# Kernel optimization log

Hardware: AMD Instinct MI355X
Metric: run time of the kernel (lower is better)

## Reference

```python
import jax, jax.numpy as jnp
import numpy as np

B, D_IN, D_H, D_F = 65536, 256, 1024, 512


def _linear_init(key, fan_in, fan_out):
    # torch.nn.Linear default: U(-1/sqrt(fan_in), 1/sqrt(fan_in))
    bound = 1.0 / np.sqrt(fan_in)
    kw, kb = jax.random.split(key)
    W = jax.random.uniform(kw, (fan_in, fan_out), minval=-bound, maxval=bound, dtype=jnp.float32)
    b = jax.random.uniform(kb, (fan_out,), minval=-bound, maxval=bound, dtype=jnp.float32)
    return W, b


def setup_inputs() -> dict:
    key = jax.random.key(0)
    ks = jax.random.split(key, 8)
    obs = jax.random.normal(ks[0], (B, D_IN), dtype=jnp.float32)
    # columns 2:4 must be one-hot: [1,0] -> expert b, [0,1] -> expert c
    tag = jax.random.randint(ks[1], (B,), 0, 2).astype(jnp.float32)
    onehot = jnp.stack([tag, 1.0 - tag], axis=1)  # [B, 2]
    obs = obs.at[:, 2:4].set(onehot)
    inp = {"obs": obs}
    for i, name in enumerate(("b", "c", "p")):
        k1, k2 = jax.random.split(ks[2 + i])
        W1, b1 = _linear_init(k1, D_IN, D_H)
        W2, b2 = _linear_init(k2, D_H, D_F)
        inp[f"W1_{name}"] = W1
        inp[f"b1_{name}"] = b1
        inp[f"W2_{name}"] = W2
        inp[f"b2_{name}"] = b2
    return inp


def _mlp(x, W1, b1, W2, b2):
    # Linear -> ReLU -> Linear (tianshou-style MLP, flatten_input=False)
    return jax.nn.relu(x @ W1 + b1) @ W2 + b2


def reference(obs, W1_b, b1_b, W2_b, b2_b, W1_c, b1_c, W2_c, b2_c, W1_p, b1_p, W2_p, b2_p):
    # Vectorized form of the per-row Python loop: compute both experts and the
    # shared branch on the full batch, then select per row by the one-hot tag.
    out_b = _mlp(obs, W1_b, b1_b, W2_b, b2_b)  # [B, D_F]
    out_c = _mlp(obs, W1_c, b1_c, W2_c, b2_c)  # [B, D_F]
    out_p = _mlp(obs, W1_p, b1_p, W2_p, b2_p)  # [B, D_F]
    is_b = (obs[:, 2:3] == 1.0) & (obs[:, 3:4] == 0.0)  # [B, 1]
    expert = jnp.where(is_b, out_b, out_c)
    return jnp.concatenate([expert, out_p], axis=-1)  # [B, 2*D_F]
```

## Files before the change

### kernel.cpp

```cpp
#include <hip/hip_runtime.h>
#include <hip/hip_bf16.h>

#define DIN 256
#define DH  1024
#define DF  512
#define NROWS 65536

#define WS_WTS   0
#define WS_PB    4718592
#define WS_PC    4980736
#define WS_CNT   5242880
#define WS_OFFS  5243904

typedef __attribute__((ext_vector_type(8))) short bf16x8;
typedef __attribute__((ext_vector_type(4))) float f32x4;

__device__ __forceinline__ unsigned short f2b(float f) {
    union { float f; unsigned u; } v; v.f = f;
    unsigned r = v.u + 0x7FFFu + ((v.u >> 16) & 1u);
    return (unsigned short)(r >> 16);
}

__device__ __forceinline__ void gll16(const void* g, void* l) {
    __builtin_amdgcn_global_load_lds(
        (const __attribute__((address_space(1))) void*)g,
        (__attribute__((address_space(3))) void*)l, 16, 0, 0);
}

__global__ __launch_bounds__(256) void transpose_to_bf16(
        const float* __restrict__ src, unsigned short* __restrict__ dst,
        int K, int N) {
    __shared__ float tile[64][65];
    int k0 = blockIdx.x * 64, n0 = blockIdx.y * 64;
    int t = threadIdx.x;
    for (int i = 0; i < 16; ++i) {
        int idx = t + i * 256;
        int kk = idx >> 6, nn = idx & 63;
        tile[kk][nn] = src[(size_t)(k0 + kk) * N + (n0 + nn)];
    }
    __syncthreads();
    for (int i = 0; i < 16; ++i) {
        int idx = t + i * 256;
        int nn = idx >> 6, kk = idx & 63;
        dst[(size_t)(n0 + nn) * K + (k0 + kk)] = f2b(tile[kk][nn]);
    }
}

__device__ __forceinline__ int row_tag(const float* obs, int row) {
    float c2 = obs[(size_t)row * DIN + 2];
    float c3 = obs[(size_t)row * DIN + 3];
    return (c2 == 1.0f && c3 == 0.0f) ? 1 : 0;
}

__global__ __launch_bounds__(256) void tag_count(const float* __restrict__ obs,
                                                 int* __restrict__ cnt) {
    int t = threadIdx.x;
    int tag = row_tag(obs, blockIdx.x * 256 + t);
    unsigned long long m = __ballot(tag);
    __shared__ int wc[4];
    if ((t & 63) == 0) wc[t >> 6] = __popcll(m);
    __syncthreads();
    if (t == 0) cnt[blockIdx.x] = wc[0] + wc[1] + wc[2] + wc[3];
}

__global__ __launch_bounds__(256) void scan256(const int* __restrict__ cnt,
                                               int* __restrict__ offs) {
    __shared__ int s[256];
    int t = threadIdx.x;
    s[t] = cnt[t];
    __syncthreads();
    for (int d = 1; d < 256; d <<= 1) {
        int v = (t >= d) ? s[t - d] : 0;
        __syncthreads();
        s[t] += v;
        __syncthreads();
    }
    offs[t] = s[t] - cnt[t];
    if (t == 255) offs[256] = s[255];
}

__global__ __launch_bounds__(256) void fill_perm(const float* __restrict__ obs,
                                                 const int* __restrict__ offs,
                                                 int* __restrict__ pb,
                                                 int* __restrict__ pc) {
    int t = threadIdx.x, bid = blockIdx.x;
    int row = bid * 256 + t;
    int tag = row_tag(obs, row);
    unsigned long long m = __ballot(tag);
    __shared__ int wc[4];
    int lane = t & 63, wv = t >> 6;
    if (lane == 0) wc[wv] = __popcll(m);
    __syncthreads();
    int woff = 0;
    for (int i = 0; i < 4; ++i) if (i < wv) woff += wc[i];
    int lb = woff + __popcll(m & ((1ull << lane) - 1ull));
    int base_b = offs[bid];
    if (tag) pb[base_b + lb] = row;
    else     pc[bid * 256 - base_b + (t - lb)] = row;
}

__global__ __launch_bounds__(512, 2) void fused_mlp(
    const float* __restrict__ obs,
    const unsigned short* __restrict__ wts,
    const int* __restrict__ perm_b, const int* __restrict__ perm_c,
    const int* __restrict__ offs,
    const float* __restrict__ b1_0, const float* __restrict__ b2_0,
    const float* __restrict__ b1_1, const float* __restrict__ b2_1,
    const float* __restrict__ b1_2, const float* __restrict__ b2_2,
    float* __restrict__ out)
{
    extern __shared__ char lds[];
    char* ldsX  = lds;
    char* ldsW1 = lds + 65536;
    char* ldsQA = lds + 98304;
    char* ldsQB = lds + 114688;
    char* ldsH  = lds + 131072;
    float* ldsB1 = (float*)(lds + 147456);
    float* ldsB2 = (float*)(lds + 151552);
    int*  ldsPr  = (int*)(lds + 153600);

    const int ob = blockIdx.x;
    const int xcd = ob & 7, ii = ob >> 3;
    const int bid = (xcd == 0) ? ii : (129 + (xcd - 1) * 128 + ii);

    int branch, base, cnt;
    const int* perm;
    if (bid < 512) {
        branch = 2; base = bid * 128; cnt = NROWS; perm = nullptr;
    } else {
        int eb = bid - 512;
        int nb = offs[256];
        int nbb = (nb + 127) >> 7;
        int nc = NROWS - nb;
        int ncb = (nc + 127) >> 7;
        if (eb < nbb)            { branch = 0; base = eb * 128;         cnt = nb; perm = perm_b; }
        else if (eb < nbb + ncb) { branch = 1; base = (eb - nbb) * 128; cnt = nc; perm = perm_c; }
        else return;
    }

    const float* b1 = branch == 0 ? b1_0 : (branch == 1 ? b1_1 : b1_2);
    const float* b2 = branch == 0 ? b2_0 : (branch == 1 ? b2_1 : b2_2);
    const char* w1t = (const char*)(wts + (size_t)branch * (DH * DIN));
    const char* w2t = (const char*)(wts + (size_t)3 * DH * DIN + (size_t)branch * (DF * DH));

    const int t = threadIdx.x;
    const int lane = t & 63;
    const int w = t >> 6;
    const int l15 = lane & 15;
    const int g = lane >> 4;

    ldsB1[t] = b1[t];
    ldsB1[t + 512] = b1[t + 512];
    ldsB2[t] = b2[t];
    if (t < 128) {
        int gr = base + t;
        ldsPr[t] = (gr < cnt) ? (perm ? perm[gr] : gr) : -1;
    }
    #pragma unroll
    for (int i = 0; i < 16; ++i) {
        int idx = t + i * 512;
        int r = idx >> 6, c4 = idx & 63;
        int gr = base + r;
        int grow = gr < cnt ? gr : cnt - 1;
        if (perm) grow = perm[grow];
        f32x4 v = *(const f32x4*)(obs + (size_t)grow * DIN + c4 * 4);
        ushort4 p4;
        p4.x = f2b(v.x); p4.y = f2b(v.y); p4.z = f2b(v.z); p4.w = f2b(v.w);
        *(ushort4*)(ldsX + r * 512 + ((c4 * 8) ^ ((r & 7) << 4))) = p4;
    }
    #pragma unroll
    for (int i = 0; i < 4; ++i) {
        int slot = t + i * 512;
        int nl = slot >> 5, boff = (slot & 31) << 4;
        gll16(w1t + (size_t)nl * 512 + (boff ^ ((nl & 7) << 4)), ldsW1 + slot * 16);
    }
    __syncthreads();

    const int rg = w & 3, cg = w >> 2;
    const int wr = w >> 2, wc = w & 3;

    const int ar0 = rg * 32 + l15, ar1 = ar0 + 16;
    const int asw0 = (ar0 & 7) << 4, asw1 = (ar1 & 7) << 4;
    const int bn0 = cg * 32 + l15, bn1 = bn0 + 16;
    const int bsw0 = (bn0 & 7) << 4, bsw1 = (bn1 & 7) << 4;

    f32x4 acc[4][8];
    #pragma unroll
    for (int a = 0; a < 4; ++a)
        #pragma unroll
        for (int b = 0; b < 8; ++b)
            #pragma unroll
            for (int e = 0; e < 4; ++e) acc[a][b][e] = 0.0f;

    #define STAGE_Q(buf, q, hc_)                                               \
        {                                                                      \
            _Pragma("unroll")                                                  \
            for (int i = 0; i < 2; ++i) {                                      \
                int slot = t + i * 512;                                        \
                int nl = slot >> 3, boff = (slot & 7) << 4;                    \
                gll16(w2t + (size_t)((q) * 128 + nl) * 2048 + (hc_) * 128      \
                          + (boff ^ ((nl & 7) << 4)),                          \
                      (buf) + slot * 16);                                      \
            }                                                                  \
        }

    #define QUARTER_MFMA(buf, c0)                                              \
        {                                                                      \
            _Pragma("unroll")                                                  \
            for (int k2 = 0; k2 < 2; ++k2)                                     \
                _Pragma("unroll")                                              \
                for (int ct = 0; ct < 2; ++ct) {                               \
                    int fr = wc * 32 + ct * 16 + l15;                          \
                    bf16x8 bb = *(const bf16x8*)((buf) + fr * 128 +            \
                                 ((k2 * 64 + g * 16) ^ ((fr & 7) << 4)));      \
                    _Pragma("unroll")                                          \
                    for (int rt = 0; rt < 4; ++rt)                             \
                        acc[rt][(c0) + ct] = __builtin_amdgcn_mfma_f32_16x16x32_bf16( \
                            hA[rt][k2], bb, acc[rt][(c0) + ct], 0, 0, 0);      \
                }                                                              \
        }

    for (int hc = 0; hc < 16; ++hc) {
        STAGE_Q(ldsQA, 0, hc);
        f32x4 aH[2][2];
        #pragma unroll
        for (int a = 0; a < 2; ++a)
            #pragma unroll
            for (int b = 0; b < 2; ++b)
                #pragma unroll
                for (int e = 0; e < 4; ++e) aH[a][b][e] = 0.0f;
        __builtin_amdgcn_s_setprio(1);
        #pragma unroll
        for (int kk = 0; kk < 8; ++kk) {
            int kb = kk * 64 + g * 16;
            bf16x8 a0 = *(const bf16x8*)(ldsX  + ar0 * 512 + (kb ^ asw0));
            bf16x8 a1 = *(const bf16x8*)(ldsX  + ar1 * 512 + (kb ^ asw1));
            bf16x8 b0 = *(const bf16x8*)(ldsW1 + bn0 * 512 + (kb ^ bsw0));
            bf16x8 b1f = *(const bf16x8*)(ldsW1 + bn1 * 512 + (kb ^ bsw1));
            aH[0][0] = __builtin_amdgcn_mfma_f32_16x16x32_bf16(a0, b0,  aH[0][0], 0, 0, 0);
            aH[0][1] = __builtin_amdgcn_mfma_f32_16x16x32_bf16(a0, b1f, aH[0][1], 0, 0, 0);
            aH[1][0] = __builtin_amdgcn_mfma_f32_16x16x32_bf16(a1, b0,  aH[1][0], 0, 0, 0);
            aH[1][1] = __builtin_amdgcn_mfma_f32_16x16x32_bf16(a1, b1f, aH[1][1], 0, 0, 0);
        }
        __builtin_amdgcn_s_setprio(0);
        {
            float b1v0 = ldsB1[hc * 64 + cg * 32 + l15];
            float b1v1 = ldsB1[hc * 64 + cg * 32 + 16 + l15];
            #pragma unroll
            for (int art = 0; art < 2; ++art)
                #pragma unroll
                for (int bct = 0; bct < 2; ++bct) {
                    int col2 = (cg * 32 + bct * 16 + l15) * 2;
                    float bv = bct ? b1v1 : b1v0;
                    #pragma unroll
                    for (int r = 0; r < 4; ++r) {
                        int hrow = rg * 32 + art * 16 + g * 4 + r;
                        float vv = fmaxf(aH[art][bct][r] + bv, 0.0f);
                        *(unsigned short*)(ldsH + hrow * 128 + (col2 ^ ((hrow & 7) << 4))) = f2b(vv);
                    }
                }
        }
        __syncthreads();

        STAGE_Q(ldsQB, 1, hc);
        bf16x8 hA[4][2];
        #pragma unroll
        for (int rt = 0; rt < 4; ++rt)
            #pragma unroll
            for (int k2 = 0; k2 < 2; ++k2) {
                int hr = wr * 64 + rt * 16 + l15;
                hA[rt][k2] = *(const bf16x8*)(ldsH + hr * 128 + ((k2 * 64 + g * 16) ^ ((hr & 7) << 4)));
            }
        __builtin_amdgcn_s_setprio(1);
        QUARTER_MFMA(ldsQA, 0);
        __builtin_amdgcn_s_setprio(0);
        __syncthreads();

        STAGE_Q(ldsQA, 2, hc);
        __builtin_amdgcn_s_setprio(1);
        QUARTER_MFMA(ldsQB, 2);
        __builtin_amdgcn_s_setprio(0);
        __syncthreads();

        STAGE_Q(ldsQB, 3, hc);
        __builtin_amdgcn_s_setprio(1);
        QUARTER_MFMA(ldsQA, 4);
        __builtin_amdgcn_s_setprio(0);
        __syncthreads();

        if (hc < 15) {
            int nchunk = hc + 1;
            #pragma unroll
            for (int i = 0; i < 4; ++i) {
                int slot = t + i * 512;
                int nl = slot >> 5, boff = (slot & 31) << 4;
                gll16(w1t + (size_t)(nchunk * 64 + nl) * 512 + (boff ^ ((nl & 7) << 4)),
                      ldsW1 + slot * 16);
            }
        }
        __builtin_amdgcn_s_setprio(1);
        QUARTER_MFMA(ldsQB, 6);
        __builtin_amdgcn_s_setprio(0);
        __syncthreads();
    }

    int colq[8]; float b2v[8];
    #pragma unroll
    for (int q = 0; q < 8; ++q) {
        colq[q] = (q >> 1) * 128 + wc * 32 + (q & 1) * 16 + l15;
        b2v[q] = ldsB2[colq[q]];
    }
    const int cb = (branch == 2) ? DF : 0;
    #pragma unroll
    for (int rt = 0; rt < 4; ++rt)
        #pragma unroll
        for (int r = 0; r < 4; ++r) {
            int row = wr * 64 + rt * 16 + g * 4 + r;
            int prow = ldsPr[row];
            if (prow >= 0) {
                float* op = out + (size_t)prow * (2 * DF) + cb;
                #pragma unroll
                for (int q = 0; q < 8; ++q)
                    op[colq[q]] = acc[rt][q][r] + b2v[q];
            }
        }
}

extern "C" void kernel_launch(void* const* d_in, const int* in_sizes, int n_in,
                              void* d_out, int out_size, void* d_ws, size_t ws_size,
                              hipStream_t stream) {
    const float* obs = (const float*)d_in[0];
    const float* W1[3] = {(const float*)d_in[1], (const float*)d_in[5], (const float*)d_in[9]};
    const float* b1[3] = {(const float*)d_in[2], (const float*)d_in[6], (const float*)d_in[10]};
    const float* W2[3] = {(const float*)d_in[3], (const float*)d_in[7], (const float*)d_in[11]};
    const float* b2[3] = {(const float*)d_in[4], (const float*)d_in[8], (const float*)d_in[12]};

    char* ws = (char*)d_ws;
    unsigned short* wts = (unsigned short*)(ws + WS_WTS);
    int* pb   = (int*)(ws + WS_PB);
    int* pc   = (int*)(ws + WS_PC);
    int* cnt  = (int*)(ws + WS_CNT);
    int* offs = (int*)(ws + WS_OFFS);

    for (int br = 0; br < 3; ++br) {
        transpose_to_bf16<<<dim3(DIN / 64, DH / 64), 256, 0, stream>>>(
            W1[br], wts + (size_t)br * DH * DIN, DIN, DH);
        transpose_to_bf16<<<dim3(DH / 64, DF / 64), 256, 0, stream>>>(
            W2[br], wts + (size_t)3 * DH * DIN + (size_t)br * DF * DH, DH, DF);
    }
    tag_count<<<256, 256, 0, stream>>>(obs, cnt);
    scan256<<<1, 256, 0, stream>>>(cnt, offs);
    fill_perm<<<256, 256, 0, stream>>>(obs, offs, pb, pc);

    hipFuncSetAttribute((const void*)fused_mlp,
                        hipFuncAttributeMaxDynamicSharedMemorySize, 154112);
    fused_mlp<<<1025, 512, 154112, stream>>>(obs, wts, pb, pc, offs,
        b1[0], b2[0], b1[1], b2[1], b1[2], b2[2], (float*)d_out);
}
```

Baseline: 376.2 us.

## Split fused MLP into hidden and output kernels staged through workspace

Replaces the single fused MLP kernel with two kernels per pass. The first computes the bf16 hidden activations into a large workspace buffer. The second reads them back and computes the output GEMM with a 128x512 tile, scattering results to the permuted rows. The shared branch and the routed experts run as separate passes over a unified row permutation. This aims to lower LDS pressure and give the second GEMM larger register tiles, at the cost of writing and re-reading the hidden buffer (about 128MB per pass) through HBM. The old fused path remains as a fallback when the workspace is too small.

Result: slower. 450.1 us (+19.6%).

```diff
diff --git a/kernel.cpp b/kernel.cpp
--- a/kernel.cpp
+++ b/kernel.cpp
@@ -11,6 +11,9 @@
 #define WS_PC    4980736
 #define WS_CNT   5242880
 #define WS_OFFS  5243904
+#define WS_U     5248000
+#define WS_H     8388608ull
+#define WS_NEED  (8388608ull + 134742016ull)
 
 typedef __attribute__((ext_vector_type(8))) short bf16x8;
 typedef __attribute__((ext_vector_type(4))) float f32x4;
@@ -97,6 +100,300 @@
     int base_b = offs[bid];
     if (tag) pb[base_b + lb] = row;
     else     pc[bid * 256 - base_b + (t - lb)] = row;
+}
+
+__global__ __launch_bounds__(256) void fill_permU(const float* __restrict__ obs,
+                                                  const int* __restrict__ offs,
+                                                  int* __restrict__ U) {
+    int t = threadIdx.x, bid = blockIdx.x;
+    int row = bid * 256 + t;
+    int tag = row_tag(obs, row);
+    unsigned long long m = __ballot(tag);
+    __shared__ int wc[4];
+    int lane = t & 63, wv = t >> 6;
+    if (lane == 0) wc[wv] = __popcll(m);
+    __syncthreads();
+    int woff = 0;
+    for (int i = 0; i < 4; ++i) if (i < wv) woff += wc[i];
+    int lb = woff + __popcll(m & ((1ull << lane) - 1ull));
+    int base_b = offs[bid];
+    int nb = offs[256];
+    if (tag) U[base_b + lb] = row;
+    else     U[nb + bid * 256 - base_b + (t - lb)] = row;
+}
+
+__global__ __launch_bounds__(512, 1) void k1_hidden(
+    const float* __restrict__ obs, const unsigned short* __restrict__ wts,
+    const int* __restrict__ U, const int* __restrict__ offs,
+    const float* __restrict__ b1_0, const float* __restrict__ b1_1,
+    const float* __restrict__ b1_2,
+    unsigned short* __restrict__ H, int mode)
+{
+    extern __shared__ char lds[];
+    char* ldsX   = lds;
+    char* ldsW1a = lds + 65536;
+    char* ldsW1b = lds + 98304;
+    float* ldsB1 = (float*)(lds + 131072);
+
+    const int bid = blockIdx.x;
+    const int nb  = offs[256];
+    const int nc  = NROWS - nb;
+    const int nbp = (nb + 127) & ~127;
+    const int ncp = (nc + 127) & ~127;
+    const int evb = bid * 128;
+    int branch;
+    if (mode == 0) branch = 2;
+    else {
+        if (evb >= nbp + ncp) return;
+        branch = (evb < nbp) ? 0 : 1;
+    }
+    const float* b1g = branch == 0 ? b1_0 : (branch == 1 ? b1_1 : b1_2);
+    const char* w1t = (const char*)(wts + (size_t)branch * (DH * DIN));
+
+    const int t = threadIdx.x;
+    const int lane = t & 63;
+    const int w = t >> 6;
+    const int l15 = lane & 15;
+    const int g = lane >> 4;
+
+    ldsB1[t] = b1g[t];
+    ldsB1[t + 512] = b1g[t + 512];
+
+    #pragma unroll
+    for (int i = 0; i < 16; ++i) {
+        int idx = t + i * 512;
+        int r = idx >> 6, c4 = idx & 63;
+        int j = evb + r;
+        int grow;
+        if (mode == 0) grow = j;
+        else if (j < nbp) grow = U[j < nb ? j : nb - 1];
+        else { int ix = j - nbp; grow = U[nb + (ix < nc ? ix : nc - 1)]; }
+        f32x4 v = *(const f32x4*)(obs + (size_t)grow * DIN + c4 * 4);
+        ushort4 p4;
+        p4.x = f2b(v.x); p4.y = f2b(v.y); p4.z = f2b(v.z); p4.w = f2b(v.w);
+        *(ushort4*)(ldsX + r * 512 + ((c4 * 8) ^ ((r & 7) << 4))) = p4;
+    }
+    #pragma unroll
+    for (int i = 0; i < 4; ++i) {
+        int slot = t + i * 512;
+        int nl = slot >> 5, boff = (slot & 31) << 4;
+        gll16(w1t + (size_t)nl * 512 + (boff ^ ((nl & 7) << 4)), ldsW1a + slot * 16);
+    }
+    __syncthreads();
+
+    const int rg = w & 3, cg = w >> 2;
+    const int ar0 = rg * 32 + l15, ar1 = ar0 + 16;
+    const int asw0 = (ar0 & 7) << 4, asw1 = (ar1 & 7) << 4;
+    const int bn0 = cg * 32 + l15, bn1 = bn0 + 16;
+    const int bsw0 = (bn0 & 7) << 4, bsw1 = (bn1 & 7) << 4;
+    const size_t hb = (size_t)bid * 128;
+
+    for (int wch = 0; wch < 16; ++wch) {
+        const char* Wc = (wch & 1) ? ldsW1b : ldsW1a;
+        if (wch < 15) {
+            char* dst = (wch & 1) ? ldsW1a : ldsW1b;
+            #pragma unroll
+            for (int i = 0; i < 4; ++i) {
+                int slot = t + i * 512;
+                int nl = slot >> 5, boff = (slot & 31) << 4;
+                gll16(w1t + (size_t)((wch + 1) * 64 + nl) * 512 + (boff ^ ((nl & 7) << 4)),
+                      dst + slot * 16);
+            }
+        }
+        f32x4 aH[2][2];
+        #pragma unroll
+        for (int a = 0; a < 2; ++a)
+            #pragma unroll
+            for (int b = 0; b < 2; ++b)
+                #pragma unroll
+                for (int e = 0; e < 4; ++e) aH[a][b][e] = 0.0f;
+        __builtin_amdgcn_s_setprio(1);
+        #pragma unroll
+        for (int kk = 0; kk < 8; ++kk) {
+            int kb = kk * 64 + g * 16;
+            bf16x8 a0  = *(const bf16x8*)(ldsX + ar0 * 512 + (kb ^ asw0));
+            bf16x8 a1  = *(const bf16x8*)(ldsX + ar1 * 512 + (kb ^ asw1));
+            bf16x8 b0  = *(const bf16x8*)(Wc + bn0 * 512 + (kb ^ bsw0));
+            bf16x8 b1f = *(const bf16x8*)(Wc + bn1 * 512 + (kb ^ bsw1));
+            aH[0][0] = __builtin_amdgcn_mfma_f32_16x16x32_bf16(a0, b0,  aH[0][0], 0, 0, 0);
+            aH[0][1] = __builtin_amdgcn_mfma_f32_16x16x32_bf16(a0, b1f, aH[0][1], 0, 0, 0);
+            aH[1][0] = __builtin_amdgcn_mfma_f32_16x16x32_bf16(a1, b0,  aH[1][0], 0, 0, 0);
+            aH[1][1] = __builtin_amdgcn_mfma_f32_16x16x32_bf16(a1, b1f, aH[1][1], 0, 0, 0);
+        }
+        __builtin_amdgcn_s_setprio(0);
+        {
+            float b1v0 = ldsB1[wch * 64 + cg * 32 + l15];
+            float b1v1 = ldsB1[wch * 64 + cg * 32 + 16 + l15];
+            #pragma unroll
+            for (int art = 0; art < 2; ++art)
+                #pragma unroll
+                for (int bct = 0; bct < 2; ++bct) {
+                    float bv = bct ? b1v1 : b1v0;
+                    int hcol = wch * 64 + cg * 32 + bct * 16 + l15;
+                    #pragma unroll
+                    for (int r = 0; r < 4; ++r) {
+                        int hrow = rg * 32 + art * 16 + g * 4 + r;
+                        float vv = fmaxf(aH[art][bct][r] + bv, 0.0f);
+                        H[(hb + hrow) * DH + hcol] = f2b(vv);
+                    }
+                }
+        }
+        __syncthreads();
+    }
+}
+
+__global__ __launch_bounds__(512, 1) void k2_out(
+    const unsigned short* __restrict__ H, const unsigned short* __restrict__ wts,
+    const int* __restrict__ U, const int* __restrict__ offs,
+    const float* __restrict__ b2_0, const float* __restrict__ b2_1,
+    const float* __restrict__ b2_2,
+    float* __restrict__ out, int mode)
+{
+    extern __shared__ char lds[];
+    char* ldsHA  = lds;
+    char* ldsHB  = lds + 16384;
+    char* ldsW2A = lds + 32768;
+    char* ldsW2B = lds + 65536;
+    float* ldsB2 = (float*)(lds + 98304);
+    int*  ldsPr  = (int*)(lds + 100352);
+
+    const int bid = blockIdx.x;
+    const int nb  = offs[256];
+    const int nc  = NROWS - nb;
+    const int nbp = (nb + 127) & ~127;
+    const int ncp = (nc + 127) & ~127;
+    const int evb = bid * 128;
+    int branch;
+    if (mode == 0) branch = 2;
+    else {
+        if (evb >= nbp + ncp) return;
+        branch = (evb < nbp) ? 0 : 1;
+    }
+    const float* b2g = branch == 0 ? b2_0 : (branch == 1 ? b2_1 : b2_2);
+    const char* w2t = (const char*)(wts + (size_t)3 * DH * DIN + (size_t)branch * (DF * DH));
+
+    const int t = threadIdx.x;
+    const int lane = t & 63;
+    const int w = t >> 6;
+    const int l15 = lane & 15;
+    const int g = lane >> 4;
+
+    ldsB2[t] = b2g[t];
+    if (t < 128) {
+        int j = evb + t;
+        int pr;
+        if (mode == 0) pr = j;
+        else if (j < nbp) pr = U[j < nb ? j : nb - 1];
+        else { int ix = j - nbp; pr = U[nb + (ix < nc ? ix : nc - 1)]; }
+        ldsPr[t] = pr;
+    }
+    const size_t hb = (size_t)bid * 128;
+
+    #pragma unroll
+    for (int i = 0; i < 2; ++i) {
+        int slot = t + i * 512;
+        int nl = slot >> 3, boff = (slot & 7) << 4;
+        gll16((const char*)H + (hb + nl) * 2048 + (boff ^ ((nl & 7) << 4)),
+              ldsHA + slot * 16);
+    }
+    #pragma unroll
+    for (int i = 0; i < 4; ++i) {
+        int slot = t + i * 512;
+        int nl = slot >> 3, boff = (slot & 7) << 4;
+        gll16(w2t + (size_t)nl * 2048 + (boff ^ ((nl & 7) << 4)), ldsW2A + slot * 16);
+    }
+    __syncthreads();
+
+    const int wr = w >> 2, wc = w & 3;
+    f32x4 acc[4][8];
+    #pragma unroll
+    for (int a = 0; a < 4; ++a)
+        #pragma unroll
+        for (int b = 0; b < 8; ++b)
+            #pragma unroll
+            for (int e = 0; e < 4; ++e) acc[a][b][e] = 0.0f;
+
+    for (int ch = 0; ch < 16; ++ch) {
+        const char* Hc = (ch & 1) ? ldsHB : ldsHA;
+        #pragma unroll
+        for (int i = 0; i < 4; ++i) {
+            int slot = t + i * 512;
+            int nl = slot >> 3, boff = (slot & 7) << 4;
+            gll16(w2t + (size_t)(256 + nl) * 2048 + ch * 128 + (boff ^ ((nl & 7) << 4)),
+                  ldsW2B + slot * 16);
+        }
+        bf16x8 hA[4][2];
+        #pragma unroll
+        for (int rt = 0; rt < 4; ++rt)
+            #pragma unroll
+            for (int k2 = 0; k2 < 2; ++k2) {
+                int hr = wr * 64 + rt * 16 + l15;
+                hA[rt][k2] = *(const bf16x8*)(Hc + hr * 128 + ((k2 * 64 + g * 16) ^ ((hr & 7) << 4)));
+            }
+        __builtin_amdgcn_s_setprio(1);
+        #pragma unroll
+        for (int k2 = 0; k2 < 2; ++k2)
+            #pragma unroll
+            for (int ct = 0; ct < 4; ++ct) {
+                int fr = wc * 64 + ct * 16 + l15;
+                bf16x8 bb = *(const bf16x8*)(ldsW2A + fr * 128 + ((k2 * 64 + g * 16) ^ ((fr & 7) << 4)));
+                #pragma unroll
+                for (int rt = 0; rt < 4; ++rt)
+                    acc[rt][ct] = __builtin_amdgcn_mfma_f32_16x16x32_bf16(hA[rt][k2], bb, acc[rt][ct], 0, 0, 0);
+            }
+        __builtin_amdgcn_s_setprio(0);
+        __syncthreads();
+
+        if (ch < 15) {
+            char* hd = (ch & 1) ? ldsHA : ldsHB;
+            #pragma unroll
+            for (int i = 0; i < 2; ++i) {
+                int slot = t + i * 512;
+                int nl = slot >> 3, boff = (slot & 7) << 4;
+                gll16((const char*)H + (hb + nl) * 2048 + (ch + 1) * 128 + (boff ^ ((nl & 7) << 4)),
+                      hd + slot * 16);
+            }
+            #pragma unroll
+            for (int i = 0; i < 4; ++i) {
+                int slot = t + i * 512;
+                int nl = slot >> 3, boff = (slot & 7) << 4;
+                gll16(w2t + (size_t)nl * 2048 + (ch + 1) * 128 + (boff ^ ((nl & 7) << 4)),
+                      ldsW2A + slot * 16);
+            }
+        }
+        __builtin_amdgcn_s_setprio(1);
+        #pragma unroll
+        for (int k2 = 0; k2 < 2; ++k2)
+            #pragma unroll
+            for (int ct = 0; ct < 4; ++ct) {
+                int fr = wc * 64 + ct * 16 + l15;
+                bf16x8 bb = *(const bf16x8*)(ldsW2B + fr * 128 + ((k2 * 64 + g * 16) ^ ((fr & 7) << 4)));
+                #pragma unroll
+                for (int rt = 0; rt < 4; ++rt)
+                    acc[rt][4 + ct] = __builtin_amdgcn_mfma_f32_16x16x32_bf16(hA[rt][k2], bb, acc[rt][4 + ct], 0, 0, 0);
+            }
+        __builtin_amdgcn_s_setprio(0);
+        __syncthreads();
+    }
+
+    const int colbase = (mode == 0) ? DF : 0;
+    int colq[8]; float b2v[8];
+    #pragma unroll
+    for (int q = 0; q < 8; ++q) {
+        colq[q] = (q >> 2) * 256 + wc * 64 + (q & 3) * 16 + l15;
+        b2v[q] = ldsB2[colq[q]];
+    }
+    #pragma unroll
+    for (int rt = 0; rt < 4; ++rt)
+        #pragma unroll
+        for (int r = 0; r < 4; ++r) {
+            int row = wr * 64 + rt * 16 + g * 4 + r;
+            int prow = ldsPr[row];
+            float* op = out + (size_t)prow * (2 * DF) + colbase;
+            #pragma unroll
+            for (int q = 0; q < 8; ++q)
+                op[colq[q]] = acc[rt][q][r] + b2v[q];
+        }
 }
 
 __global__ __launch_bounds__(512, 2) void fused_mlp(
@@ -341,6 +638,8 @@
     int* pc   = (int*)(ws + WS_PC);
     int* cnt  = (int*)(ws + WS_CNT);
     int* offs = (int*)(ws + WS_OFFS);
+    int* U    = (int*)(ws + WS_U);
+    unsigned short* Hws = (unsigned short*)(ws + WS_H);
 
     for (int br = 0; br < 3; ++br) {
         transpose_to_bf16<<<dim3(DIN / 64, DH / 64), 256, 0, stream>>>(
@@ -350,10 +649,26 @@
     }
     tag_count<<<256, 256, 0, stream>>>(obs, cnt);
     scan256<<<1, 256, 0, stream>>>(cnt, offs);
-    fill_perm<<<256, 256, 0, stream>>>(obs, offs, pb, pc);
-
-    hipFuncSetAttribute((const void*)fused_mlp,
-                        hipFuncAttributeMaxDynamicSharedMemorySize, 154112);
-    fused_mlp<<<1025, 512, 154112, stream>>>(obs, wts, pb, pc, offs,
-        b1[0], b2[0], b1[1], b2[1], b1[2], b2[2], (float*)d_out);
-}
+
+    if (ws_size >= WS_NEED) {
+        fill_permU<<<256, 256, 0, stream>>>(obs, offs, U);
+        hipFuncSetAttribute((const void*)k1_hidden,
+                            hipFuncAttributeMaxDynamicSharedMemorySize, 135168);
+        hipFuncSetAttribute((const void*)k2_out,
+                            hipFuncAttributeMaxDynamicSharedMemorySize, 100864);
+        k1_hidden<<<512, 512, 135168, stream>>>(obs, wts, U, offs,
+            b1[0], b1[1], b1[2], Hws, 0);
+        k2_out<<<512, 512, 100864, stream>>>(Hws, wts, U, offs,
+            b2[0], b2[1], b2[2], (float*)d_out, 0);
+        k1_hidden<<<514, 512, 135168, stream>>>(obs, wts, U, offs,
+            b1[0], b1[1], b1[2], Hws, 1);
+        k2_out<<<514, 512, 100864, stream>>>(Hws, wts, U, offs,
+            b2[0], b2[1], b2[2], (float*)d_out, 1);
+    } else {
+        fill_perm<<<256, 256, 0, stream>>>(obs, offs, pb, pc);
+        hipFuncSetAttribute((const void*)fused_mlp,
+                            hipFuncAttributeMaxDynamicSharedMemorySize, 154112);
+        fused_mlp<<<1025, 512, 154112, stream>>>(obs, wts, pb, pc, offs,
+            b1[0], b2[0], b1[1], b2[1], b1[2], b2[2], (float*)d_out);
+    }
+}
```

## Shrink fused MLP block to 4 waves with larger per-wave output tiles

Applied to the files above, without the earlier changes.

Cuts the fused MLP workgroup from 512 to 256 threads. Each wave now owns a 32-row strip in the first GEMM and a 32-column slice across all 128 rows in the second, so the acc tile doubles to 8x8 fragments. Staging loops are widened to cover the same LDS data with fewer threads. This raises register use per wave and halves the waves available to hide latency, in exchange for more MFMA work per LDS fragment load.

Result: slower. 1.081 ms (+187.3%).

```diff
diff --git a/kernel.cpp b/kernel.cpp
--- a/kernel.cpp
+++ b/kernel.cpp
@@ -99,7 +99,7 @@
     else     pc[bid * 256 - base_b + (t - lb)] = row;
 }
 
-__global__ __launch_bounds__(512, 2) void fused_mlp(
+__global__ __launch_bounds__(256, 1) void fused_mlp(
     const float* __restrict__ obs,
     const unsigned short* __restrict__ wts,
     const int* __restrict__ perm_b, const int* __restrict__ perm_c,
@@ -150,15 +150,18 @@
     const int g = lane >> 4;
 
     ldsB1[t] = b1[t];
+    ldsB1[t + 256] = b1[t + 256];
     ldsB1[t + 512] = b1[t + 512];
+    ldsB1[t + 768] = b1[t + 768];
     ldsB2[t] = b2[t];
+    ldsB2[t + 256] = b2[t + 256];
     if (t < 128) {
         int gr = base + t;
         ldsPr[t] = (gr < cnt) ? (perm ? perm[gr] : gr) : -1;
     }
     #pragma unroll
-    for (int i = 0; i < 16; ++i) {
-        int idx = t + i * 512;
+    for (int i = 0; i < 32; ++i) {
+        int idx = t + i * 256;
         int r = idx >> 6, c4 = idx & 63;
         int gr = base + r;
         int grow = gr < cnt ? gr : cnt - 1;
@@ -169,24 +172,19 @@
         *(ushort4*)(ldsX + r * 512 + ((c4 * 8) ^ ((r & 7) << 4))) = p4;
     }
     #pragma unroll
-    for (int i = 0; i < 4; ++i) {
-        int slot = t + i * 512;
+    for (int i = 0; i < 8; ++i) {
+        int slot = t + i * 256;
         int nl = slot >> 5, boff = (slot & 31) << 4;
         gll16(w1t + (size_t)nl * 512 + (boff ^ ((nl & 7) << 4)), ldsW1 + slot * 16);
     }
     __syncthreads();
 
-    const int rg = w & 3, cg = w >> 2;
-    const int wr = w >> 2, wc = w & 3;
-
-    const int ar0 = rg * 32 + l15, ar1 = ar0 + 16;
+    const int ar0 = w * 32 + l15, ar1 = ar0 + 16;
     const int asw0 = (ar0 & 7) << 4, asw1 = (ar1 & 7) << 4;
-    const int bn0 = cg * 32 + l15, bn1 = bn0 + 16;
-    const int bsw0 = (bn0 & 7) << 4, bsw1 = (bn1 & 7) << 4;
-
-    f32x4 acc[4][8];
-    #pragma unroll
-    for (int a = 0; a < 4; ++a)
+
+    f32x4 acc[8][8];
+    #pragma unroll
+    for (int a = 0; a < 8; ++a)
         #pragma unroll
         for (int b = 0; b < 8; ++b)
             #pragma unroll
@@ -195,8 +193,8 @@
     #define STAGE_Q(buf, q, hc_)                                               \
         {                                                                      \
             _Pragma("unroll")                                                  \
-            for (int i = 0; i < 2; ++i) {                                      \
-                int slot = t + i * 512;                                        \
+            for (int i = 0; i < 4; ++i) {                                      \
+                int slot = t + i * 256;                                        \
                 int nl = slot >> 3, boff = (slot & 7) << 4;                    \
                 gll16(w2t + (size_t)((q) * 128 + nl) * 2048 + (hc_) * 128      \
                           + (boff ^ ((nl & 7) << 4)),                          \
@@ -204,72 +202,71 @@
             }                                                                  \
         }
 
-    #define QUARTER_MFMA(buf, c0)                                              \
+    #define QUARTER_MFMA(buf, q)                                               \
         {                                                                      \
             _Pragma("unroll")                                                  \
             for (int k2 = 0; k2 < 2; ++k2)                                     \
                 _Pragma("unroll")                                              \
-                for (int ct = 0; ct < 2; ++ct) {                               \
-                    int fr = wc * 32 + ct * 16 + l15;                          \
+                for (int cf = 0; cf < 2; ++cf) {                               \
+                    int fr = w * 32 + cf * 16 + l15;                           \
                     bf16x8 bb = *(const bf16x8*)((buf) + fr * 128 +            \
                                  ((k2 * 64 + g * 16) ^ ((fr & 7) << 4)));      \
                     _Pragma("unroll")                                          \
-                    for (int rt = 0; rt < 4; ++rt)                             \
-                        acc[rt][(c0) + ct] = __builtin_amdgcn_mfma_f32_16x16x32_bf16( \
-                            hA[rt][k2], bb, acc[rt][(c0) + ct], 0, 0, 0);      \
+                    for (int rf = 0; rf < 8; ++rf)                             \
+                        acc[rf][(q) * 2 + cf] = __builtin_amdgcn_mfma_f32_16x16x32_bf16( \
+                            hA[rf][k2], bb, acc[rf][(q) * 2 + cf], 0, 0, 0);   \
                 }                                                              \
         }
 
     for (int hc = 0; hc < 16; ++hc) {
         STAGE_Q(ldsQA, 0, hc);
-        f32x4 aH[2][2];
+        f32x4 aH[2][4];
         #pragma unroll
         for (int a = 0; a < 2; ++a)
             #pragma unroll
-            for (int b = 0; b < 2; ++b)
+            for (int b = 0; b < 4; ++b)
                 #pragma unroll
                 for (int e = 0; e < 4; ++e) aH[a][b][e] = 0.0f;
         __builtin_amdgcn_s_setprio(1);
         #pragma unroll
         for (int kk = 0; kk < 8; ++kk) {
             int kb = kk * 64 + g * 16;
-            bf16x8 a0 = *(const bf16x8*)(ldsX  + ar0 * 512 + (kb ^ asw0));
-            bf16x8 a1 = *(const bf16x8*)(ldsX  + ar1 * 512 + (kb ^ asw1));
-            bf16x8 b0 = *(const bf16x8*)(ldsW1 + bn0 * 512 + (kb ^ bsw0));
-            bf16x8 b1f = *(const bf16x8*)(ldsW1 + bn1 * 512 + (kb ^ bsw1));
-            aH[0][0] = __builtin_amdgcn_mfma_f32_16x16x32_bf16(a0, b0,  aH[0][0], 0, 0, 0);
-            aH[0][1] = __builtin_amdgcn_mfma_f32_16x16x32_bf16(a0, b1f, aH[0][1], 0, 0, 0);
-            aH[1][0] = __builtin_amdgcn_mfma_f32_16x16x32_bf16(a1, b0,  aH[1][0], 0, 0, 0);
-            aH[1][1] = __builtin_amdgcn_mfma_f32_16x16x32_bf16(a1, b1f, aH[1][1], 0, 0, 0);
+            bf16x8 a0 = *(const bf16x8*)(ldsX + ar0 * 512 + (kb ^ asw0));
+            bf16x8 a1 = *(const bf16x8*)(ldsX + ar1 * 512 + (kb ^ asw1));
+            #pragma unroll
+            for (int bct = 0; bct < 4; ++bct) {
+                int bn = bct * 16 + l15;
+                bf16x8 bf = *(const bf16x8*)(ldsW1 + bn * 512 + (kb ^ ((bn & 7) << 4)));
+                aH[0][bct] = __builtin_amdgcn_mfma_f32_16x16x32_bf16(a0, bf, aH[0][bct], 0, 0, 0);
+                aH[1][bct] = __builtin_amdgcn_mfma_f32_16x16x32_bf16(a1, bf, aH[1][bct], 0, 0, 0);
+            }
         }
         __builtin_amdgcn_s_setprio(0);
         {
-            float b1v0 = ldsB1[hc * 64 + cg * 32 + l15];
-            float b1v1 = ldsB1[hc * 64 + cg * 32 + 16 + l15];
-            #pragma unroll
-            for (int art = 0; art < 2; ++art)
+            #pragma unroll
+            for (int bct = 0; bct < 4; ++bct) {
+                float bv = ldsB1[hc * 64 + bct * 16 + l15];
+                int col2 = (bct * 16 + l15) * 2;
                 #pragma unroll
-                for (int bct = 0; bct < 2; ++bct) {
-                    int col2 = (cg * 32 + bct * 16 + l15) * 2;
-                    float bv = bct ? b1v1 : b1v0;
+                for (int art = 0; art < 2; ++art)
                     #pragma unroll
                     for (int r = 0; r < 4; ++r) {
-                        int hrow = rg * 32 + art * 16 + g * 4 + r;
+                        int hrow = w * 32 + art * 16 + g * 4 + r;
                         float vv = fmaxf(aH[art][bct][r] + bv, 0.0f);
                         *(unsigned short*)(ldsH + hrow * 128 + (col2 ^ ((hrow & 7) << 4))) = f2b(vv);
                     }
-                }
+            }
         }
         __syncthreads();
 
         STAGE_Q(ldsQB, 1, hc);
-        bf16x8 hA[4][2];
-        #pragma unroll
-        for (int rt = 0; rt < 4; ++rt)
+        bf16x8 hA[8][2];
+        #pragma unroll
+        for (int rf = 0; rf < 8; ++rf)
             #pragma unroll
             for (int k2 = 0; k2 < 2; ++k2) {
-                int hr = wr * 64 + rt * 16 + l15;
-                hA[rt][k2] = *(const bf16x8*)(ldsH + hr * 128 + ((k2 * 64 + g * 16) ^ ((hr & 7) << 4)));
+                int hr = rf * 16 + l15;
+                hA[rf][k2] = *(const bf16x8*)(ldsH + hr * 128 + ((k2 * 64 + g * 16) ^ ((hr & 7) << 4)));
             }
         __builtin_amdgcn_s_setprio(1);
         QUARTER_MFMA(ldsQA, 0);
@@ -278,50 +275,50 @@
 
         STAGE_Q(ldsQA, 2, hc);
         __builtin_amdgcn_s_setprio(1);
-        QUARTER_MFMA(ldsQB, 2);
+        QUARTER_MFMA(ldsQB, 1);
         __builtin_amdgcn_s_setprio(0);
         __syncthreads();
 
         STAGE_Q(ldsQB, 3, hc);
         __builtin_amdgcn_s_setprio(1);
-        QUARTER_MFMA(ldsQA, 4);
+        QUARTER_MFMA(ldsQA, 2);
         __builtin_amdgcn_s_setprio(0);
         __syncthreads();
 
         if (hc < 15) {
             int nchunk = hc + 1;
             #pragma unroll
-            for (int i = 0; i < 4; ++i) {
-                int slot = t + i * 512;
+            for (int i = 0; i < 8; ++i) {
+                int slot = t + i * 256;
                 int nl = slot >> 5, boff = (slot & 31) << 4;
                 gll16(w1t + (size_t)(nchunk * 64 + nl) * 512 + (boff ^ ((nl & 7) << 4)),
                       ldsW1 + slot * 16);
             }
         }
         __builtin_amdgcn_s_setprio(1);
-        QUARTER_MFMA(ldsQB, 6);
+        QUARTER_MFMA(ldsQB, 3);
         __builtin_amdgcn_s_setprio(0);
         __syncthreads();
     }
 
     int colq[8]; float b2v[8];
     #pragma unroll
-    for (int q = 0; q < 8; ++q) {
-        colq[q] = (q >> 1) * 128 + wc * 32 + (q & 1) * 16 + l15;
-        b2v[q] = ldsB2[colq[q]];
+    for (int cc = 0; cc < 8; ++cc) {
+        colq[cc] = (cc >> 1) * 128 + w * 32 + (cc & 1) * 16 + l15;
+        b2v[cc] = ldsB2[colq[cc]];
     }
     const int cb = (branch == 2) ? DF : 0;
     #pragma unroll
-    for (int rt = 0; rt < 4; ++rt)
+    for (int rf = 0; rf < 8; ++rf)
         #pragma unroll
         for (int r = 0; r < 4; ++r) {
-            int row = wr * 64 + rt * 16 + g * 4 + r;
+            int row = rf * 16 + g * 4 + r;
             int prow = ldsPr[row];
             if (prow >= 0) {
                 float* op = out + (size_t)prow * (2 * DF) + cb;
                 #pragma unroll
-                for (int q = 0; q < 8; ++q)
-                    op[colq[q]] = acc[rt][q][r] + b2v[q];
+                for (int cc = 0; cc < 8; ++cc)
+                    op[colq[cc]] = acc[rf][cc][r] + b2v[cc];
             }
         }
 }
@@ -354,6 +351,6 @@
 
     hipFuncSetAttribute((const void*)fused_mlp,
                         hipFuncAttributeMaxDynamicSharedMemorySize, 154112);
-    fused_mlp<<<1025, 512, 154112, stream>>>(obs, wts, pb, pc, offs,
+    fused_mlp<<<1025, 256, 154112, stream>>>(obs, wts, pb, pc, offs,
         b1[0], b2[0], b1[1], b2[1], b1[2], b2[2], (float*)d_out);
 }
```

## Pipeline W1/W2 staging with partial vmcnt barriers across chunk iterations

Applied to the files above, without the earlier changes.

Replaces __syncthreads with inline-asm barriers that wait only on older global-to-LDS loads (partial vmcnt), so newer prefetches stay in flight across barriers. The W2 quarter-0 load and the next W1 chunk are issued one stage earlier, in the previous iteration, so they overlap the MFMA work instead of sitting on the critical path at the start of each chunk. The risk is correctness: the vmcnt counts must match the exact number of loads outstanding per thread. The final iteration also issues redundant wrapped-around prefetches, which are drained before the epilogue.

Result: faster. 341.8 us (-9.1%).

```diff
diff --git a/kernel.cpp b/kernel.cpp
--- a/kernel.cpp
+++ b/kernel.cpp
@@ -26,6 +26,9 @@
         (const __attribute__((address_space(1))) void*)g,
         (__attribute__((address_space(3))) void*)l, 16, 0, 0);
 }
+
+#define BAR_V(N) asm volatile("s_waitcnt vmcnt(" #N ") lgkmcnt(0)\ns_barrier" ::: "memory")
+#define DRAIN_VM() asm volatile("s_waitcnt vmcnt(0)" ::: "memory")
 
 __global__ __launch_bounds__(256) void transpose_to_bf16(
         const float* __restrict__ src, unsigned short* __restrict__ dst,
@@ -168,29 +171,7 @@
         p4.x = f2b(v.x); p4.y = f2b(v.y); p4.z = f2b(v.z); p4.w = f2b(v.w);
         *(ushort4*)(ldsX + r * 512 + ((c4 * 8) ^ ((r & 7) << 4))) = p4;
     }
-    #pragma unroll
-    for (int i = 0; i < 4; ++i) {
-        int slot = t + i * 512;
-        int nl = slot >> 5, boff = (slot & 31) << 4;
-        gll16(w1t + (size_t)nl * 512 + (boff ^ ((nl & 7) << 4)), ldsW1 + slot * 16);
-    }
-    __syncthreads();
-
-    const int rg = w & 3, cg = w >> 2;
-    const int wr = w >> 2, wc = w & 3;
-
-    const int ar0 = rg * 32 + l15, ar1 = ar0 + 16;
-    const int asw0 = (ar0 & 7) << 4, asw1 = (ar1 & 7) << 4;
-    const int bn0 = cg * 32 + l15, bn1 = bn0 + 16;
-    const int bsw0 = (bn0 & 7) << 4, bsw1 = (bn1 & 7) << 4;
-
-    f32x4 acc[4][8];
-    #pragma unroll
-    for (int a = 0; a < 4; ++a)
-        #pragma unroll
-        for (int b = 0; b < 8; ++b)
-            #pragma unroll
-            for (int e = 0; e < 4; ++e) acc[a][b][e] = 0.0f;
+    DRAIN_VM();
 
     #define STAGE_Q(buf, q, hc_)                                               \
         {                                                                      \
@@ -203,6 +184,37 @@
                       (buf) + slot * 16);                                      \
             }                                                                  \
         }
+
+    #define STAGE_W1(hc_)                                                      \
+        {                                                                      \
+            _Pragma("unroll")                                                  \
+            for (int i = 0; i < 4; ++i) {                                      \
+                int slot = t + i * 512;                                        \
+                int nl = slot >> 5, boff = (slot & 31) << 4;                   \
+                gll16(w1t + (size_t)((hc_) * 64 + nl) * 512 + (boff ^ ((nl & 7) << 4)), \
+                      ldsW1 + slot * 16);                                      \
+            }                                                                  \
+        }
+
+    STAGE_W1(0);
+    STAGE_Q(ldsQA, 0, 0);
+    BAR_V(2);
+
+    const int rg = w & 3, cg = w >> 2;
+    const int wr = w >> 2, wc = w & 3;
+
+    const int ar0 = rg * 32 + l15, ar1 = ar0 + 16;
+    const int asw0 = (ar0 & 7) << 4, asw1 = (ar1 & 7) << 4;
+    const int bn0 = cg * 32 + l15, bn1 = bn0 + 16;
+    const int bsw0 = (bn0 & 7) << 4, bsw1 = (bn1 & 7) << 4;
+
+    f32x4 acc[4][8];
+    #pragma unroll
+    for (int a = 0; a < 4; ++a)
+        #pragma unroll
+        for (int b = 0; b < 8; ++b)
+            #pragma unroll
+            for (int e = 0; e < 4; ++e) acc[a][b][e] = 0.0f;
 
     #define QUARTER_MFMA(buf, c0)                                              \
         {                                                                      \
@@ -221,7 +233,7 @@
         }
 
     for (int hc = 0; hc < 16; ++hc) {
-        STAGE_Q(ldsQA, 0, hc);
+        STAGE_Q(ldsQB, 1, hc);
         f32x4 aH[2][2];
         #pragma unroll
         for (int a = 0; a < 2; ++a)
@@ -260,9 +272,8 @@
                     }
                 }
         }
-        __syncthreads();
-
-        STAGE_Q(ldsQB, 1, hc);
+        BAR_V(2);
+
         bf16x8 hA[4][2];
         #pragma unroll
         for (int rt = 0; rt < 4; ++rt)
@@ -274,35 +285,28 @@
         __builtin_amdgcn_s_setprio(1);
         QUARTER_MFMA(ldsQA, 0);
         __builtin_amdgcn_s_setprio(0);
-        __syncthreads();
+        BAR_V(0);
 
         STAGE_Q(ldsQA, 2, hc);
         __builtin_amdgcn_s_setprio(1);
         QUARTER_MFMA(ldsQB, 2);
         __builtin_amdgcn_s_setprio(0);
-        __syncthreads();
+        BAR_V(0);
 
         STAGE_Q(ldsQB, 3, hc);
+        STAGE_W1((hc + 1) & 15);
         __builtin_amdgcn_s_setprio(1);
         QUARTER_MFMA(ldsQA, 4);
         __builtin_amdgcn_s_setprio(0);
-        __syncthreads();
-
-        if (hc < 15) {
-            int nchunk = hc + 1;
-            #pragma unroll
-            for (int i = 0; i < 4; ++i) {
-                int slot = t + i * 512;
-                int nl = slot >> 5, boff = (slot & 31) << 4;
-                gll16(w1t + (size_t)(nchunk * 64 + nl) * 512 + (boff ^ ((nl & 7) << 4)),
-                      ldsW1 + slot * 16);
-            }
-        }
+        BAR_V(4);
+
+        STAGE_Q(ldsQA, 0, (hc + 1) & 15);
         __builtin_amdgcn_s_setprio(1);
         QUARTER_MFMA(ldsQB, 6);
         __builtin_amdgcn_s_setprio(0);
-        __syncthreads();
-    }
+        BAR_V(2);
+    }
+    DRAIN_VM();
 
     int colq[8]; float b2v[8];
     #pragma unroll
```
